# Performance work log

Measured on AMD Instinct MI355X. Metric: run time of the kernel, lower is better.

## Reference

```python
import jax, jax.numpy as jnp
import numpy as np

# dims
B, LP, CIN, AUX = 8, 1024, 64, 32
COUT, OUT_LEN = 64, 512
DM, DI, NS, PH, NH = 1024, 2048, 16, 64, 32  # d_model, d_inner, d_state, headdim, n_heads
NL, PATCH, KPRE, KCONV = 4, 8, 5, 4
GG, KH, CHUNK = 8, 2048, 64  # kan grid, kan hidden, chunk_size
DIN = 2 * DI + 2 * NS + NH   # in_proj output: z, xBC, dt
CONV_DIM = DI + 2 * NS


def _conv1d(x, w, b, stride, pad_l, pad_r, groups=1):
    # x: [B, C, L], w: [O, I/groups, K]
    y = jax.lax.conv_general_dilated(x, w, (stride,), [(pad_l, pad_r)],
                                     dimension_numbers=("NCH", "OIH", "NCH"),
                                     feature_group_count=groups)
    return y + b[None, :, None]


def _rmsnorm(x, w):
    return x * jax.lax.rsqrt(jnp.mean(x * x, axis=-1, keepdims=True) + 1e-5) * w


def _mamba(u, in_w, conv_w, conv_b, A_log, Dh, dt_bias, out_w):
    # Mamba2-style selective SSM block (bias-free projections, causal depthwise conv).
    Bs, L, _ = u.shape
    zxbcdt = jnp.einsum("bld,ed->ble", u, in_w)  # [B,L,DIN]
    z = zxbcdt[..., :DI]
    xBC = zxbcdt[..., DI:DI + CONV_DIM]
    dt = jax.nn.softplus(zxbcdt[..., DI + CONV_DIM:] + dt_bias)  # [B,L,NH]
    xBC = jax.nn.silu(_conv1d(xBC.transpose(0, 2, 1), conv_w, conv_b, 1, KCONV - 1, 0,
                              groups=CONV_DIM)).transpose(0, 2, 1)
    xh = xBC[..., :DI].reshape(Bs, L, NH, PH)
    Bm = xBC[..., DI:DI + NS]   # [B,L,NS]
    Cm = xBC[..., DI + NS:]     # [B,L,NS]
    dA = jnp.exp(-jnp.exp(A_log) * dt)  # [B,L,NH]

    def step(s, t):
        x_t, B_t, C_t, dA_t, dt_t = t
        s = s * dA_t[:, :, None, None] + jnp.einsum("bhp,bn,bh->bhpn", x_t, B_t, dt_t)
        return s, jnp.einsum("bhpn,bn->bhp", s, C_t)

    s0 = jnp.zeros((Bs, NH, PH, NS), u.dtype)
    xs = (xh.transpose(1, 0, 2, 3), Bm.transpose(1, 0, 2), Cm.transpose(1, 0, 2),
          dA.transpose(1, 0, 2), dt.transpose(1, 0, 2))
    _, ys = jax.lax.scan(step, s0, xs)  # ys: [L,B,NH,PH]
    y = ys.transpose(1, 0, 2, 3) + xh * Dh[None, None, :, None]
    y = y.reshape(Bs, L, DI) * jax.nn.silu(z)
    return jnp.einsum("ble,de->bld", y, out_w)


def _kan(x, log_bw, base_w, base_b, spline_w):
    # Gaussian-basis KAN layer: base Linear + spline Linear over RBF expansion.
    grid = jnp.linspace(-2.0, 2.0, GG)
    bw = jnp.exp(log_bw)[None] + 1e-6                 # [1,in,1]
    basis = jnp.exp(-((x[..., None] - grid[None, None, :]) ** 2) / (2.0 * bw * bw))
    return x @ base_w.T + base_b + basis.reshape(x.shape[0], -1) @ spline_w.T


def setup_inputs() -> dict:
    ks = iter(jax.random.split(jax.random.key(0), 64))
    nrm = lambda shape, s=0.02: jax.random.normal(next(ks), shape, jnp.float32) * s
    inp = {"x_prefix": jax.random.normal(next(ks), (B, LP, CIN), jnp.float32),
           "y_aux": jax.random.normal(next(ks), (B, AUX), jnp.float32),
           "pre_conv_w": nrm((DM, CIN, KPRE), 0.1), "pre_conv_b": jnp.zeros((DM,)),
           "patch_w": nrm((DM, DM, PATCH), 0.05), "patch_b": jnp.zeros((DM,))}
    for pre in ("fwd", "bwd"):
        inp[pre + "_norm_w"] = jnp.ones((NL, DM))
        inp[pre + "_in_w"] = nrm((NL, DIN, DM))
        inp[pre + "_conv_w"] = nrm((NL, CONV_DIM, 1, KCONV), 0.1)
        inp[pre + "_conv_b"] = jnp.zeros((NL, CONV_DIM))
        inp[pre + "_A_log"] = jnp.zeros((NL, NH))
        inp[pre + "_D"] = jnp.ones((NL, NH))
        inp[pre + "_dt_bias"] = nrm((NL, NH), 0.5)
        inp[pre + "_out_w"] = nrm((NL, DM, DI))
    inp.update(aux_w=nrm((DM, AUX)), aux_b=jnp.zeros((DM,)),
               kan1_log_bw=jnp.zeros((3 * DM, 1)), kan1_base_w=nrm((KH, 3 * DM)),
               kan1_base_b=jnp.zeros((KH,)), kan1_spline_w=nrm((KH, 3 * DM * GG), 0.005),
               kan2_log_bw=jnp.zeros((KH, 1)), kan2_base_w=nrm((DM, KH)),
               kan2_base_b=jnp.zeros((DM,)), kan2_spline_w=nrm((DM, KH * GG), 0.005),
               shared_w=nrm((DM, DM)), shared_b=jnp.zeros((DM,)),
               heads_w=nrm((COUT, OUT_LEN, DM)), heads_b=jnp.zeros((COUT, OUT_LEN)))
    return inp


def reference(x_prefix, y_aux, pre_conv_w, pre_conv_b, patch_w, patch_b,
              fwd_norm_w, fwd_in_w, fwd_conv_w, fwd_conv_b, fwd_A_log, fwd_D, fwd_dt_bias, fwd_out_w,
              bwd_norm_w, bwd_in_w, bwd_conv_w, bwd_conv_b, bwd_A_log, bwd_D, bwd_dt_bias, bwd_out_w,
              aux_w, aux_b, kan1_log_bw, kan1_base_w, kan1_base_b, kan1_spline_w,
              kan2_log_bw, kan2_base_w, kan2_base_b, kan2_spline_w,
              shared_w, shared_b, heads_w, heads_b):
    # encode_prefix
    x = jax.nn.silu(_conv1d(x_prefix.transpose(0, 2, 1), pre_conv_w, pre_conv_b, 1, KPRE // 2, KPRE // 2))
    x = _conv1d(x, patch_w, patch_b, PATCH, 0, 0).transpose(0, 2, 1)  # [B, 128, DM]
    rem = x.shape[1] % CHUNK
    if rem:
        x = jnp.pad(x, ((0, 0), (0, CHUNK - rem), (0, 0)))
    h_f, h_b = x, x[:, ::-1]
    for i in range(NL):
        h_f = h_f + _mamba(_rmsnorm(h_f, fwd_norm_w[i]), fwd_in_w[i], fwd_conv_w[i], fwd_conv_b[i],
                           fwd_A_log[i], fwd_D[i], fwd_dt_bias[i], fwd_out_w[i])
        h_b = h_b + _mamba(_rmsnorm(h_b, bwd_norm_w[i]), bwd_in_w[i], bwd_conv_w[i], bwd_conv_b[i],
                           bwd_A_log[i], bwd_D[i], bwd_dt_bias[i], bwd_out_w[i])
    ctx = jnp.concatenate([h_f.mean(1), h_b[:, ::-1].mean(1)], axis=-1)  # [B, 2*DM]
    # fusion + heads
    aux = jax.nn.silu(y_aux @ aux_w.T + aux_b)
    fused = jnp.concatenate([ctx, aux], axis=-1)  # [B, 3*DM]
    fused = jax.nn.silu(_kan(fused, kan1_log_bw, kan1_base_w, kan1_base_b, kan1_spline_w))
    fused = jax.nn.silu(_kan(fused, kan2_log_bw, kan2_base_w, kan2_base_b, kan2_spline_w))
    fused = jax.nn.silu(fused @ shared_w.T + shared_b)
    # all channel heads fused into one batched GEMM: [B, OUT_LEN, COUT]
    return jnp.einsum("bd,cld->blc", fused, heads_w) + heads_b.T[None]
```

## Files before the change

### kernel.cpp

```cpp
#include <hip/hip_runtime.h>
#include <hip/hip_bf16.h>
#include <math.h>

#define B_    8
#define LP_   1024
#define CIN_  64
#define DM_   1024
#define DI_   2048
#define NS_   16
#define PH_   64
#define NH_   32
#define NL_   4
#define GG_   8
#define KH_   2048
#define DIN_  4160
#define NPAD_ 4224
#define CONVD_ 2080
#define L_    128
#define R_    1024
#define OUTL_ 512
#define COUT_ 64

typedef __bf16 bf16x8 __attribute__((ext_vector_type(8)));
typedef float f32x4 __attribute__((ext_vector_type(4)));
typedef unsigned short ushort;

__device__ __forceinline__ float silu_f(float x) { return x / (1.0f + expf(-x)); }

__device__ __forceinline__ ushort f2bu(float x) {
    union { __hip_bfloat16 h; ushort u; } c; c.h = __float2bfloat16(x); return c.u;
}
__device__ __forceinline__ float bu2f(ushort u) {
    union { ushort u; __hip_bfloat16 h; } c; c.u = u; return __bfloat162float(c.h);
}

__device__ __forceinline__ void gload_lds16(const void* g, void* l) {
    __builtin_amdgcn_global_load_lds((const __attribute__((address_space(1))) unsigned int*)g,
                                     (__attribute__((address_space(3))) unsigned int*)l, 16, 0, 0);
}

__device__ __forceinline__ float merge2(float a, float b, int mask, int lane) {
    float x = (lane & mask) ? b : a;
    float y = (lane & mask) ? a : b;
    return x + __shfl_xor(y, mask);
}
__device__ __forceinline__ float reduce8(float* a, int lane) {
    float c0 = merge2(a[0], a[1], 1, lane);
    float c1 = merge2(a[2], a[3], 1, lane);
    float c2 = merge2(a[4], a[5], 1, lane);
    float c3 = merge2(a[6], a[7], 1, lane);
    float d0 = merge2(c0, c1, 2, lane);
    float d1 = merge2(c2, c3, 2, lane);
    float e  = merge2(d0, d1, 4, lane);
    e += __shfl_xor(e, 8);
    e += __shfl_xor(e, 16);
    e += __shfl_xor(e, 32);
    return e;
}

#define CVT_IN_T4  1081344
#define CVT_OUT_T4 524288
#define CVT_PER    1605632
#define CVT_TOT    12845056
#define PREP_W1 327680
#define PREP_W2 8388608
#define PREP_W3 2621440
#define PREP_TOT 11337728
__global__ __launch_bounds__(256) void k_cvt_prep(
    const float* __restrict__ in0, const float* __restrict__ in1,
    const float* __restrict__ o0, const float* __restrict__ o1,
    __hip_bfloat16* __restrict__ wBBa, __hip_bfloat16* __restrict__ wOBa,
    const float* __restrict__ pre_w, const float* __restrict__ patch_w, const float* __restrict__ xp,
    __hip_bfloat16* __restrict__ wpreT, __hip_bfloat16* __restrict__ wpatchT, __hip_bfloat16* __restrict__ Apre)
{
    int gi = blockIdx.x * 256 + threadIdx.x;
    if (gi < CVT_TOT) {
        int ld = gi / CVT_PER;
        int r = gi - ld * CVT_PER;
        int l = ld >> 1, d = ld & 1;
        const float* inw  = (d ? in1 : in0) + (size_t)l * DIN_ * DM_;
        const float* outw = (d ? o1 : o0) + (size_t)l * DM_ * DI_;
        if (r < CVT_IN_T4) {
            int idx = r * 4; int row = idx >> 10;
            __hip_bfloat16* dst = wBBa + (size_t)ld * NPAD_ * 1024 + idx;
            if (row < DIN_) {
                float4 v = *(const float4*)(inw + idx);
                dst[0] = __float2bfloat16(v.x); dst[1] = __float2bfloat16(v.y);
                dst[2] = __float2bfloat16(v.z); dst[3] = __float2bfloat16(v.w);
            } else {
                dst[0] = __float2bfloat16(0.f); dst[1] = __float2bfloat16(0.f);
                dst[2] = __float2bfloat16(0.f); dst[3] = __float2bfloat16(0.f);
            }
        } else {
            int idx = (r - CVT_IN_T4) * 4;
            __hip_bfloat16* dst = wOBa + (size_t)ld * 2048 * 1024 + idx;
            float4 v = *(const float4*)(outw + idx);
            dst[0] = __float2bfloat16(v.x); dst[1] = __float2bfloat16(v.y);
            dst[2] = __float2bfloat16(v.z); dst[3] = __float2bfloat16(v.w);
        }
        return;
    }
    int idx = gi - CVT_TOT;
    if (idx < PREP_W1) {
        int d = idx / 320, kk = idx % 320;
        int kp = kk >> 6, c = kk & 63;
        wpreT[idx] = __float2bfloat16(pre_w[(d * CIN_ + c) * 5 + kp]);
    } else if (idx < PREP_W1 + PREP_W2) {
        int i = idx - PREP_W1;
        int d = i >> 13, kk = i & 8191;
        int kp = kk >> 10, din = kk & 1023;
        wpatchT[i] = __float2bfloat16(patch_w[((size_t)d << 13) + din * 8 + kp]);
    } else if (idx < PREP_TOT) {
        int i = idx - PREP_W1 - PREP_W2;
        int kk = i % 320; int r = i / 320;
        int l = r & 1023, b = r >> 10;
        int kp = kk >> 6, c = kk & 63;
        int lp = l + kp - 2;
        float v = 0.f;
        if (lp >= 0 && lp < LP_) v = xp[((size_t)b * LP_ + lp) * CIN_ + c];
        Apre[i] = __float2bfloat16(v);
    }
}

template<int BM, int BN>
__global__ __launch_bounds__(512) void k_gemm_mfma(
    const ushort* __restrict__ A, const ushort* __restrict__ B,
    const float* __restrict__ bias,
    float* __restrict__ Cf, __hip_bfloat16* __restrict__ Cb,
    int Kc, int ldk, int ldc, int Nstore, int act, int nsplit,
    long sA, long sB, long sC)
{
    constexpr int BK = 32;
    constexpr int WM = 64, WN = 32;
    constexpr int MR = WM / 16, NR = WN / 16;
    constexpr int ACH = BM * 4, BCH = BN * 4;
    __shared__ ushort sAs[2][BM * BK];
    __shared__ ushort sBs[2][BN * BK];
    int tid = threadIdx.x;
    int lane = tid & 63, w = tid >> 6;
    int wr = w >> 2, wc = w & 3;
    int z = blockIdx.z;
    int dir = z / nsplit, ks = z - dir * nsplit;
    int kbase = ks * Kc;
    int H = blockIdx.y * gridDim.x + blockIdx.x;
    int nwg = gridDim.x * gridDim.y;
    int chunk = nwg >> 3;
    int Lid = (H & 7) * chunk + (H >> 3);
    int bx = Lid / gridDim.y;
    int by = Lid - bx * gridDim.y;
    int m0 = by * BM, n0 = bx * BN;
    const ushort* Az = A + (size_t)dir * sA + kbase;
    const ushort* Bz = B + (size_t)dir * sB + kbase;

    auto STAGE = [&](int buf, int k0) {
        #pragma unroll
        for (int c = tid; c < ACH; c += 512) {
            int row = c >> 2, gp = c & 3;
            int g = gp ^ ((row >> 1) & 3);
            gload_lds16(Az + (size_t)(m0 + row) * ldk + k0 + g * 8, (char*)&sAs[buf][0] + c * 16);
        }
        #pragma unroll
        for (int c = tid; c < BCH; c += 512) {
            int row = c >> 2, gp = c & 3;
            int g = gp ^ ((row >> 1) & 3);
            gload_lds16(Bz + (size_t)(n0 + row) * ldk + k0 + g * 8, (char*)&sBs[buf][0] + c * 16);
        }
    };

    const int gsw = (((lane >> 4) ^ ((lane >> 1) & 3)) * 8);

    f32x4 acc[MR][NR] = {};
    const int NT = Kc / BK;
    STAGE(0, 0);
    __syncthreads();
    int cur = 0;
    for (int t = 0; t < NT; ++t) {
        if (t + 1 < NT) STAGE(cur ^ 1, (t + 1) * BK);
        bf16x8 af[MR], bfr[NR];
        #pragma unroll
        for (int m = 0; m < MR; ++m)
            af[m] = *(const bf16x8*)&sAs[cur][(wr * WM + m * 16 + (lane & 15)) * BK + gsw];
        #pragma unroll
        for (int n = 0; n < NR; ++n)
            bfr[n] = *(const bf16x8*)&sBs[cur][(wc * WN + n * 16 + (lane & 15)) * BK + gsw];
        #pragma unroll
        for (int m = 0; m < MR; ++m)
            #pragma unroll
            for (int n = 0; n < NR; ++n)
                acc[m][n] = __builtin_amdgcn_mfma_f32_16x16x32_bf16(af[m], bfr[n], acc[m][n], 0, 0, 0);
        __syncthreads();
        cur ^= 1;
    }
    #pragma unroll
    for (int m = 0; m < MR; ++m) {
        int row = m0 + wr * WM + m * 16 + (lane >> 4) * 4;
        #pragma unroll
        for (int n = 0; n < NR; ++n) {
            int col = n0 + wc * WN + n * 16 + (lane & 15);
            if (col < Nstore) {
                if (act == 2) {
                    float* Cfz = Cf + (size_t)z * sC;
                    #pragma unroll
                    for (int j = 0; j < 4; ++j)
                        Cfz[(size_t)(row + j) * ldc + col] = acc[m][n][j];
                } else {
                    __hip_bfloat16* Cbz = Cb + (size_t)dir * sC;
                    float bv = bias ? bias[col] : 0.f;
                    #pragma unroll
                    for (int j = 0; j < 4; ++j) {
                        float v = acc[m][n][j] + bv;
                        if (act == 1) v = silu_f(v);
                        Cbz[(size_t)(row + j) * ldc + col] = __float2bfloat16(v);
                    }
                }
            }
        }
    }
}

__global__ __launch_bounds__(256) void k_patch_fin_rms(const float* __restrict__ part, const float* __restrict__ bias,
                                                       const float* __restrict__ w0, const float* __restrict__ w1,
                                                       float* __restrict__ hf, float* __restrict__ hb,
                                                       __hip_bfloat16* __restrict__ uB) {
    int r = blockIdx.x;
    int t = threadIdx.x;
    int c = t * 4;
    float4 o = *(const float4*)(bias + c);
    #pragma unroll
    for (int s = 0; s < 8; ++s) {
        float4 v = *(const float4*)(part + (size_t)s * 1048576 + ((size_t)r << 10) + c);
        o.x += v.x; o.y += v.y; o.z += v.z; o.w += v.w;
    }
    *(float4*)(hf + ((size_t)r << 10) + c) = o;
    int rb = r ^ 127;
    *(float4*)(hb + ((size_t)rb << 10) + c) = o;
    float ss = o.x * o.x + o.y * o.y + o.z * o.z + o.w * o.w;
    #pragma unroll
    for (int of = 32; of; of >>= 1) ss += __shfl_xor(ss, of);
    __shared__ float sred[4];
    if ((t & 63) == 0) sred[t >> 6] = ss;
    __syncthreads();
    float tot = sred[0] + sred[1] + sred[2] + sred[3];
    float scale = rsqrtf(tot * (1.0f / DM_) + 1e-5f);
    float4 wf = *(const float4*)(w0 + c);
    float4 wb = *(const float4*)(w1 + c);
    __hip_bfloat16* uf = uB + ((size_t)r << 10) + c;
    __hip_bfloat16* ub = uB + ((size_t)(1024 + rb) << 10) + c;
    uf[0] = __float2bfloat16(o.x * scale * wf.x); uf[1] = __float2bfloat16(o.y * scale * wf.y);
    uf[2] = __float2bfloat16(o.z * scale * wf.z); uf[3] = __float2bfloat16(o.w * scale * wf.w);
    ub[0] = __float2bfloat16(o.x * scale * wb.x); ub[1] = __float2bfloat16(o.y * scale * wb.y);
    ub[2] = __float2bfloat16(o.z * scale * wb.z); ub[3] = __float2bfloat16(o.w * scale * wb.w);
}

template<bool DO_RMS>
__global__ __launch_bounds__(256) void k_oproj_fin_rms(const float* __restrict__ part,
                                                       const float* __restrict__ w0, const float* __restrict__ w1,
                                                       float* __restrict__ h, __hip_bfloat16* __restrict__ uB) {
    int row = blockIdx.x;
    int t = threadIdx.x;
    int c = t * 4;
    const float* p = part + (size_t)(row >> 10) * 4194304 + (size_t)(row & 1023) * 1024 + c;
    float4 o = *(const float4*)(h + ((size_t)row << 10) + c);
    #pragma unroll
    for (int s = 0; s < 4; ++s) {
        float4 v = *(const float4*)(p + (size_t)s * 1048576);
        o.x += v.x; o.y += v.y; o.z += v.z; o.w += v.w;
    }
    *(float4*)(h + ((size_t)row << 10) + c) = o;
    if (DO_RMS) {
        float ss = o.x * o.x + o.y * o.y + o.z * o.z + o.w * o.w;
        #pragma unroll
        for (int of = 32; of; of >>= 1) ss += __shfl_xor(ss, of);
        __shared__ float sred[4];
        if ((t & 63) == 0) sred[t >> 6] = ss;
        __syncthreads();
        float tot = sred[0] + sred[1] + sred[2] + sred[3];
        float scale = rsqrtf(tot * (1.0f / DM_) + 1e-5f);
        const float* w = (row >> 10) ? w1 : w0;
        float4 wv = *(const float4*)(w + c);
        __hip_bfloat16* u = uB + ((size_t)row << 10) + c;
        u[0] = __float2bfloat16(o.x * scale * wv.x); u[1] = __float2bfloat16(o.y * scale * wv.y);
        u[2] = __float2bfloat16(o.z * scale * wv.z); u[3] = __float2bfloat16(o.w * scale * wv.w);
    }
}

__global__ __launch_bounds__(256) void k_scan(const __hip_bfloat16* __restrict__ zx,
                                              const float* __restrict__ cw0, const float* __restrict__ cw1,
                                              const float* __restrict__ cb0, const float* __restrict__ cb1,
                                              const float* __restrict__ dtb0, const float* __restrict__ dtb1,
                                              const float* __restrict__ al0, const float* __restrict__ al1,
                                              const float* __restrict__ D0, const float* __restrict__ D1,
                                              __hip_bfloat16* __restrict__ ys) {
    __shared__ float xs[L_ * PH_];
    __shared__ float Bsh[L_ * NS_];
    __shared__ float Csh[L_ * NS_];
    __shared__ float dts[L_];
    __shared__ float dAs[L_];
    int bx = blockIdx.x;
    int dir = bx >> 8, b = (bx >> 5) & 7, h = bx & 31;
    const __hip_bfloat16* zxd = zx + (size_t)dir * 1024 * DIN_;
    const float* cw = dir ? cw1 : cw0;
    const float* cb = dir ? cb1 : cb0;
    const float* dt_bias = dir ? dtb1 : dtb0;
    const float* A_log   = dir ? al1 : al0;
    const float* Dh      = dir ? D1 : D0;
    __hip_bfloat16* ysd  = ys + (size_t)dir * 1024 * DI_;
    int t = threadIdx.x;
    for (int i = t; i < 2048; i += 256) {
        int l = i >> 4, p4 = i & 15;
        int cc = h * PH_ + p4 * 4;
        float a0 = cb[cc + 0], a1 = cb[cc + 1], a2 = cb[cc + 2], a3 = cb[cc + 3];
        #pragma unroll
        for (int k = 0; k < 4; ++k) {
            int lp = l - 3 + k;
            if (lp >= 0) {
                ushort4 raw = *(const ushort4*)(zxd + (size_t)(b * L_ + lp) * DIN_ + DI_ + cc);
                a0 += bu2f(raw.x) * cw[(cc + 0) * 4 + k];
                a1 += bu2f(raw.y) * cw[(cc + 1) * 4 + k];
                a2 += bu2f(raw.z) * cw[(cc + 2) * 4 + k];
                a3 += bu2f(raw.w) * cw[(cc + 3) * 4 + k];
            }
        }
        float* xp = &xs[l * PH_ + p4 * 4];
        xp[0] = silu_f(a0); xp[1] = silu_f(a1); xp[2] = silu_f(a2); xp[3] = silu_f(a3);
    }
    for (int i = t; i < 1024; i += 256) {
        int l = i >> 3, q4 = i & 7;
        int cc = DI_ + q4 * 4;
        float a0 = cb[cc + 0], a1 = cb[cc + 1], a2 = cb[cc + 2], a3 = cb[cc + 3];
        #pragma unroll
        for (int k = 0; k < 4; ++k) {
            int lp = l - 3 + k;
            if (lp >= 0) {
                ushort4 raw = *(const ushort4*)(zxd + (size_t)(b * L_ + lp) * DIN_ + DI_ + cc);
                a0 += bu2f(raw.x) * cw[(cc + 0) * 4 + k];
                a1 += bu2f(raw.y) * cw[(cc + 1) * 4 + k];
                a2 += bu2f(raw.z) * cw[(cc + 2) * 4 + k];
                a3 += bu2f(raw.w) * cw[(cc + 3) * 4 + k];
            }
        }
        float r0 = silu_f(a0), r1 = silu_f(a1), r2 = silu_f(a2), r3 = silu_f(a3);
        if (q4 < 4) {
            float* bp = &Bsh[l * NS_ + q4 * 4];
            bp[0] = r0; bp[1] = r1; bp[2] = r2; bp[3] = r3;
        } else {
            float* cp = &Csh[l * NS_ + (q4 - 4) * 4];
            cp[0] = r0; cp[1] = r1; cp[2] = r2; cp[3] = r3;
        }
    }
    if (t < L_) {
        float v = bu2f(*(const ushort*)(zxd + (size_t)(b * L_ + t) * DIN_ + 4128 + h)) + dt_bias[h];
        float sp = v > 20.f ? v : log1pf(expf(v));
        dts[t] = sp;
        dAs[t] = expf(-expf(A_log[h]) * sp);
    }
    __syncthreads();
    int p = t >> 2, n0 = (t & 3) * 4;
    float Dv = Dh[h];
    float s0 = 0.f, s1 = 0.f, s2 = 0.f, s3 = 0.f;
    for (int l = 0; l < L_; ++l) {
        float x = xs[l * 64 + p];
        float dAv = dAs[l];
        float xdt = x * dts[l];
        s0 = s0 * dAv + xdt * Bsh[l * 16 + n0 + 0];
        s1 = s1 * dAv + xdt * Bsh[l * 16 + n0 + 1];
        s2 = s2 * dAv + xdt * Bsh[l * 16 + n0 + 2];
        s3 = s3 * dAv + xdt * Bsh[l * 16 + n0 + 3];
        float cp = s0 * Csh[l * 16 + n0 + 0] + s1 * Csh[l * 16 + n0 + 1]
                 + s2 * Csh[l * 16 + n0 + 2] + s3 * Csh[l * 16 + n0 + 3];
        cp += __shfl_xor(cp, 1);
        cp += __shfl_xor(cp, 2);
        if ((t & 3) == 0) xs[l * 64 + p] = cp + x * Dv;
    }
    __syncthreads();
    for (int i = t; i < L_ * PH_; i += 256) {
        int l = i >> 6, pp = i & 63;
        float z = bu2f(*(const ushort*)(zxd + (size_t)(b * L_ + l) * DIN_ + h * PH_ + pp));
        ysd[((size_t)(b * L_ + l)) * DI_ + h * PH_ + pp] = __float2bfloat16(xs[i] * silu_f(z));
    }
}

__device__ __forceinline__ void emit_basis(float v, float lbw, float* __restrict__ bas, size_t base) {
    float bw = expf(lbw) + 1e-6f;
    float inv = 1.0f / (2.0f * bw * bw);
    #pragma unroll
    for (int g = 0; g < GG_; ++g) {
        float gg = -2.0f + g * (4.0f / 7.0f);
        float df = v - gg;
        bas[base + g] = expf(-df * df * inv);
    }
}

__global__ __launch_bounds__(256) void k_meanctx_aux(const float* __restrict__ hf, const float* __restrict__ hb,
                                                     const float* __restrict__ y_aux, const float* __restrict__ aux_w,
                                                     const float* __restrict__ aux_b, const float* __restrict__ k1_lbw,
                                                     float* __restrict__ fused, float* __restrict__ bas1) {
    int bx = blockIdx.x;
    int t = threadIdx.x;
    if (bx < 64) {
        int b = bx >> 3, ch = bx & 7;
        int d4 = t & 31, lg = t >> 5;
        int d = ch * 128 + d4 * 4;
        float4 sf = {0,0,0,0}, sb = {0,0,0,0};
        for (int l = lg; l < L_; l += 8) {
            float4 a = *(const float4*)(hf + ((size_t)b * L_ + l) * DM_ + d);
            float4 c = *(const float4*)(hb + ((size_t)b * L_ + l) * DM_ + d);
            sf.x += a.x; sf.y += a.y; sf.z += a.z; sf.w += a.w;
            sb.x += c.x; sb.y += c.y; sb.z += c.z; sb.w += c.w;
        }
        __shared__ float rf[8][128], rb[8][128];
        *(float4*)&rf[lg][d4 * 4] = sf;
        *(float4*)&rb[lg][d4 * 4] = sb;
        __syncthreads();
        if (t < 128) {
            float s1 = 0.f, s2 = 0.f;
            #pragma unroll
            for (int g = 0; g < 8; ++g) { s1 += rf[g][t]; s2 += rb[g][t]; }
            s1 *= (1.f / L_); s2 *= (1.f / L_);
            int d1 = ch * 128 + t, d2 = DM_ + ch * 128 + t;
            fused[b * 3072 + d1] = s1;
            fused[b * 3072 + d2] = s2;
            emit_basis(s1, k1_lbw[d1], bas1, ((size_t)b * 3072 + d1) * GG_);
            emit_basis(s2, k1_lbw[d2], bas1, ((size_t)b * 3072 + d2) * GG_);
        }
    } else {
        int j = (bx - 64) * 256 + t;
        if (j >= DM_) return;
        for (int b = 0; b < B_; ++b) {
            float acc = aux_b[j];
            for (int a = 0; a < 32; ++a) acc += y_aux[b * 32 + a] * aux_w[j * 32 + a];
            float v = silu_f(acc);
            int d3 = 2 * DM_ + j;
            fused[b * 3072 + d3] = v;
            emit_basis(v, k1_lbw[d3], bas1, ((size_t)b * 3072 + d3) * GG_);
        }
    }
}

template<int MODE>
__global__ __launch_bounds__(256) void k_dotk(const float* __restrict__ Wsp, const float* __restrict__ Xsp, int Ksp,
                                              const float* __restrict__ Wb, const float* __restrict__ Xb, int Kb,
                                              const float* __restrict__ bias, float* __restrict__ out,
                                              int nsp, int nch, int Dout) {
    __shared__ float sX[8][1024];
    int ch = blockIdx.y;
    bool sp = (ch < nsp);
    const float* W = sp ? Wsp : Wb;
    const float* X = sp ? Xsp : Xb;
    int K = sp ? Ksp : Kb;
    int k0 = (sp ? ch : ch - nsp) * 1024;
    int tid = threadIdx.x;
    for (int i = tid; i < 2048; i += 256) {
        int b = i >> 8, kk = (i & 255) * 4;
        *(float4*)&sX[b][kk] = *(const float4*)(X + (size_t)b * K + k0 + kk);
    }
    __syncthreads();
    int wv = tid >> 6, lane = tid & 63;
    int rowBase = blockIdx.x * 32 + wv * 8;
    for (int j = 0; j < 8; ++j) {
        int row = rowBase + j;
        const float* wr = W + (size_t)row * K + k0;
        float acc[8] = {};
        #pragma unroll
        for (int it = 0; it < 4; ++it) {
            int k = it * 256 + lane * 4;
            float4 wvv = *(const float4*)(wr + k);
            #pragma unroll
            for (int b = 0; b < 8; ++b) {
                float4 xv = *(const float4*)&sX[b][k];
                acc[b] += wvv.x * xv.x + wvv.y * xv.y + wvv.z * xv.z + wvv.w * xv.w;
            }
        }
        float e = reduce8(acc, lane);
        if (lane < 8) {
            if (MODE == 0) {
                out[((size_t)row * nch + ch) * 8 + lane] = e;
            } else if (MODE == 1) {
                out[(size_t)lane * Dout + row] = silu_f(e + bias[row]);
            } else {
                int c = row >> 9, l = row & 511;
                out[((size_t)lane * OUTL_ + l) * COUT_ + c] = e + bias[row];
            }
        }
    }
}

__global__ __launch_bounds__(256) void k_fin1_basis2(const float* __restrict__ partial, const float* __restrict__ bb,
                                                     const float* __restrict__ k2_lbw,
                                                     float* __restrict__ k1, float* __restrict__ bas2) {
    int row = blockIdx.x * 256 + threadIdx.x;
    if (row >= 2048) return;
    float bbv = bb[row];
    float lb = expf(k2_lbw[row]) + 1e-6f;
    float inv = 1.0f / (2.0f * lb * lb);
    #pragma unroll
    for (int b = 0; b < 8; ++b) {
        float s = bbv;
        #pragma unroll
        for (int c = 0; c < 27; ++c) s += partial[((size_t)row * 27 + c) * 8 + b];
        float v = silu_f(s);
        k1[(size_t)b * 2048 + row] = v;
        #pragma unroll
        for (int g = 0; g < GG_; ++g) {
            float gg = -2.0f + g * (4.0f / 7.0f);
            float df = v - gg;
            bas2[((size_t)b * 2048 + row) * GG_ + g] = expf(-df * df * inv);
        }
    }
}

template<int NCH>
__global__ __launch_bounds__(256) void k_dot_fin(const float* __restrict__ partial, const float* __restrict__ base_b,
                                                 float* __restrict__ out, int Dout) {
    int row = blockIdx.x * 256 + threadIdx.x;
    if (row >= Dout) return;
    float bb = base_b[row];
    #pragma unroll
    for (int b = 0; b < 8; ++b) {
        float s = bb;
        #pragma unroll
        for (int c = 0; c < NCH; ++c) s += partial[((size_t)row * NCH + c) * 8 + b];
        out[(size_t)b * Dout + row] = silu_f(s);
    }
}

extern "C" void kernel_launch(void* const* d_in, const int* in_sizes, int n_in,
                              void* d_out, int out_size, void* d_ws, size_t ws_size,
                              hipStream_t stream) {
    const float* x_prefix = (const float*)d_in[0];
    const float* y_aux    = (const float*)d_in[1];
    const float* pre_w    = (const float*)d_in[2];
    const float* pre_b    = (const float*)d_in[3];
    const float* patch_w  = (const float*)d_in[4];
    const float* patch_b  = (const float*)d_in[5];
    const float* norm_w[2] = {(const float*)d_in[6],  (const float*)d_in[14]};
    const float* in_w[2]   = {(const float*)d_in[7],  (const float*)d_in[15]};
    const float* conv_w[2] = {(const float*)d_in[8],  (const float*)d_in[16]};
    const float* conv_b[2] = {(const float*)d_in[9],  (const float*)d_in[17]};
    const float* A_log[2]  = {(const float*)d_in[10], (const float*)d_in[18]};
    const float* Dvec[2]   = {(const float*)d_in[11], (const float*)d_in[19]};
    const float* dt_b[2]   = {(const float*)d_in[12], (const float*)d_in[20]};
    const float* out_w[2]  = {(const float*)d_in[13], (const float*)d_in[21]};
    const float* aux_w = (const float*)d_in[22];
    const float* aux_b = (const float*)d_in[23];
    const float* k1_lbw = (const float*)d_in[24];
    const float* k1_bw  = (const float*)d_in[25];
    const float* k1_bb  = (const float*)d_in[26];
    const float* k1_sw  = (const float*)d_in[27];
    const float* k2_lbw = (const float*)d_in[28];
    const float* k2_bw  = (const float*)d_in[29];
    const float* k2_bb  = (const float*)d_in[30];
    const float* k2_sw  = (const float*)d_in[31];
    const float* sh_w = (const float*)d_in[32];
    const float* sh_b = (const float*)d_in[33];
    const float* hw   = (const float*)d_in[34];
    const float* hbias= (const float*)d_in[35];
    float* ws = (float*)d_ws;
    float* out = (float*)d_out;

    const size_t o_ApreB   = 0;
    const size_t o_wpreTB  = 1310720;
    const size_t o_x1B     = 1474560;
    const size_t o_wpatchTB= 5668864;
    const size_t o_uB   = 0;
    const size_t o_zxB  = 1048576;
    const size_t o_ysB  = 5308416;
    const size_t o_hf   = 9863168;
    const size_t o_hb   = 10911744;
    const size_t o_wBBa = 11960320;
    const size_t o_wOBa = 29261824;
    const size_t o_spart= 37650432;
    const size_t total_f = 46039040;
    const size_t o_f1   = 0;
    const size_t o_bas1 = 24576;
    const size_t o_k1   = 221184;
    const size_t o_bas2 = 237568;
    const size_t o_k2   = 368640;
    const size_t o_f4   = 376832;
    const size_t o_part = 385024;
    if (ws_size < total_f * sizeof(float)) return;

    __hip_bfloat16* ApreB   = (__hip_bfloat16*)(ws + o_ApreB);
    __hip_bfloat16* wpreTB  = (__hip_bfloat16*)(ws + o_wpreTB);
    __hip_bfloat16* x1B     = (__hip_bfloat16*)(ws + o_x1B);
    __hip_bfloat16* wpatchTB= (__hip_bfloat16*)(ws + o_wpatchTB);
    __hip_bfloat16* uB      = (__hip_bfloat16*)(ws + o_uB);
    __hip_bfloat16* zxB     = (__hip_bfloat16*)(ws + o_zxB);
    __hip_bfloat16* ysB     = (__hip_bfloat16*)(ws + o_ysB);
    __hip_bfloat16* wBBa    = (__hip_bfloat16*)(ws + o_wBBa);
    __hip_bfloat16* wOBa    = (__hip_bfloat16*)(ws + o_wOBa);
    float* hf = ws + o_hf;
    float* hb = ws + o_hb;

    k_cvt_prep<<<(CVT_TOT + PREP_TOT + 255) / 256, 256, 0, stream>>>(
        in_w[0], in_w[1], out_w[0], out_w[1], wBBa, wOBa,
        pre_w, patch_w, x_prefix, wpreTB, wpatchTB, ApreB);
    k_gemm_mfma<128,128><<<dim3(8, 64, 1), 512, 0, stream>>>(
        (const ushort*)ApreB, (const ushort*)wpreTB, pre_b, nullptr, x1B,
        320, 320, 1024, 1024, 1, 1, 0, 0, 0);
    k_gemm_mfma<128,128><<<dim3(8, 8, 8), 512, 0, stream>>>(
        (const ushort*)x1B, (const ushort*)wpatchTB, nullptr, ws + o_spart, nullptr,
        1024, 8192, 1024, 1024, 2, 8, 0, 0, (long)1024 * 1024);
    k_patch_fin_rms<<<1024, 256, 0, stream>>>(ws + o_spart, patch_b, norm_w[0], norm_w[1], hf, hb, uB);

    for (int i = 0; i < NL_; ++i) {
        k_gemm_mfma<128,128><<<dim3(33, 8, 2), 512, 0, stream>>>(
            (const ushort*)uB, (const ushort*)(wBBa + (size_t)i * 2 * NPAD_ * 1024), nullptr, nullptr, zxB,
            1024, 1024, DIN_, DIN_, 0, 1, (long)1024 * 1024, (long)NPAD_ * 1024, (long)1024 * DIN_);
        k_scan<<<512, 256, 0, stream>>>(zxB,
            conv_w[0] + (size_t)i * CONVD_ * 4, conv_w[1] + (size_t)i * CONVD_ * 4,
            conv_b[0] + (size_t)i * CONVD_, conv_b[1] + (size_t)i * CONVD_,
            dt_b[0] + i * NH_, dt_b[1] + i * NH_, A_log[0] + i * NH_, A_log[1] + i * NH_,
            Dvec[0] + i * NH_, Dvec[1] + i * NH_, ysB);
        k_gemm_mfma<128,128><<<dim3(8, 8, 8), 512, 0, stream>>>(
            (const ushort*)ysB, (const ushort*)(wOBa + (size_t)i * 2 * 2048 * 1024), nullptr, ws + o_spart, nullptr,
            512, 2048, 1024, 1024, 2, 4, (long)1024 * 2048, (long)2048 * 1024, (long)1024 * 1024);
        if (i + 1 < NL_) {
            k_oproj_fin_rms<true><<<2048, 256, 0, stream>>>(ws + o_spart,
                norm_w[0] + (size_t)(i + 1) * DM_, norm_w[1] + (size_t)(i + 1) * DM_, hf, uB);
        } else {
            k_oproj_fin_rms<false><<<2048, 256, 0, stream>>>(ws + o_spart, nullptr, nullptr, hf, nullptr);
        }
    }

    k_meanctx_aux<<<68, 256, 0, stream>>>(hf, hb, y_aux, aux_w, aux_b, k1_lbw, ws + o_f1, ws + o_bas1);
    k_dotk<0><<<dim3(64, 27), 256, 0, stream>>>(k1_sw, ws + o_bas1, 24576, k1_bw, ws + o_f1, 3072,
                                                nullptr, ws + o_part, 24, 27, 2048);
    k_fin1_basis2<<<8, 256, 0, stream>>>(ws + o_part, k1_bb, k2_lbw, ws + o_k1, ws + o_bas2);
    k_dotk<0><<<dim3(32, 18), 256, 0, stream>>>(k2_sw, ws + o_bas2, 16384, k2_bw, ws + o_k1, 2048,
                                                nullptr, ws + o_part, 16, 18, 1024);
    k_dot_fin<18><<<4, 256, 0, stream>>>(ws + o_part, k2_bb, ws + o_k2, 1024);
    k_dotk<1><<<dim3(32, 1), 256, 0, stream>>>(nullptr, nullptr, 0, sh_w, ws + o_k2, 1024,
                                               sh_b, ws + o_f4, 0, 1, 1024);
    k_dotk<2><<<dim3(1024, 1), 256, 0, stream>>>(nullptr, nullptr, 0, hw, ws + o_f4, 1024,
                                                 hbias, out, 0, 1, 32768);
}
```

Measured before the change: 836.3 us.

## Fuse fp32-to-bf16 weight conversion into Mamba projection GEMM B-tile loads

Removes the upfront pass that converted all in_proj and out_proj weights to padded bf16 buffers. The GEMM gains a BF32 mode: B tiles are read as fp32 into registers, bounds-checked against the row count instead of relying on padding, then converted and written to LDS after the MFMAs, overlapping with compute. This drops a large weight read/write pass and cuts workspace, but the GEMMs now read twice the B bytes through registers rather than async global-to-LDS copies.

After: 852.4 us. About the same (+1.9%).

```diff
diff --git a/kernel.cpp b/kernel.cpp
--- a/kernel.cpp
+++ b/kernel.cpp
@@ -14,7 +14,6 @@
 #define GG_   8
 #define KH_   2048
 #define DIN_  4160
-#define NPAD_ 4224
 #define CONVD_ 2080
 #define L_    128
 #define R_    1024
@@ -58,49 +57,15 @@
     return e;
 }
 
-#define CVT_IN_T4  1081344
-#define CVT_OUT_T4 524288
-#define CVT_PER    1605632
-#define CVT_TOT    12845056
 #define PREP_W1 327680
 #define PREP_W2 8388608
 #define PREP_W3 2621440
 #define PREP_TOT 11337728
-__global__ __launch_bounds__(256) void k_cvt_prep(
-    const float* __restrict__ in0, const float* __restrict__ in1,
-    const float* __restrict__ o0, const float* __restrict__ o1,
-    __hip_bfloat16* __restrict__ wBBa, __hip_bfloat16* __restrict__ wOBa,
+__global__ __launch_bounds__(256) void k_prep(
     const float* __restrict__ pre_w, const float* __restrict__ patch_w, const float* __restrict__ xp,
     __hip_bfloat16* __restrict__ wpreT, __hip_bfloat16* __restrict__ wpatchT, __hip_bfloat16* __restrict__ Apre)
 {
-    int gi = blockIdx.x * 256 + threadIdx.x;
-    if (gi < CVT_TOT) {
-        int ld = gi / CVT_PER;
-        int r = gi - ld * CVT_PER;
-        int l = ld >> 1, d = ld & 1;
-        const float* inw  = (d ? in1 : in0) + (size_t)l * DIN_ * DM_;
-        const float* outw = (d ? o1 : o0) + (size_t)l * DM_ * DI_;
-        if (r < CVT_IN_T4) {
-            int idx = r * 4; int row = idx >> 10;
-            __hip_bfloat16* dst = wBBa + (size_t)ld * NPAD_ * 1024 + idx;
-            if (row < DIN_) {
-                float4 v = *(const float4*)(inw + idx);
-                dst[0] = __float2bfloat16(v.x); dst[1] = __float2bfloat16(v.y);
-                dst[2] = __float2bfloat16(v.z); dst[3] = __float2bfloat16(v.w);
-            } else {
-                dst[0] = __float2bfloat16(0.f); dst[1] = __float2bfloat16(0.f);
-                dst[2] = __float2bfloat16(0.f); dst[3] = __float2bfloat16(0.f);
-            }
-        } else {
-            int idx = (r - CVT_IN_T4) * 4;
-            __hip_bfloat16* dst = wOBa + (size_t)ld * 2048 * 1024 + idx;
-            float4 v = *(const float4*)(outw + idx);
-            dst[0] = __float2bfloat16(v.x); dst[1] = __float2bfloat16(v.y);
-            dst[2] = __float2bfloat16(v.z); dst[3] = __float2bfloat16(v.w);
-        }
-        return;
-    }
-    int idx = gi - CVT_TOT;
+    int idx = blockIdx.x * 256 + threadIdx.x;
     if (idx < PREP_W1) {
         int d = idx / 320, kk = idx % 320;
         int kp = kk >> 6, c = kk & 63;
@@ -122,18 +87,18 @@
     }
 }
 
-template<int BM, int BN>
+template<int BM, int BN, int BF32>
 __global__ __launch_bounds__(512) void k_gemm_mfma(
-    const ushort* __restrict__ A, const ushort* __restrict__ B,
+    const ushort* __restrict__ A, const ushort* __restrict__ Bb,
+    const float* __restrict__ Bf0, const float* __restrict__ Bf1,
     const float* __restrict__ bias,
     float* __restrict__ Cf, __hip_bfloat16* __restrict__ Cb,
-    int Kc, int ldk, int ldc, int Nstore, int act, int nsplit,
-    long sA, long sB, long sC)
+    int Kc, int ldkA, int ldkB, int ldc, int Nstore, int act, int nsplit, int Nb,
+    long sA, long sC)
 {
     constexpr int BK = 32;
     constexpr int WM = 64, WN = 32;
     constexpr int MR = WM / 16, NR = WN / 16;
-    constexpr int ACH = BM * 4, BCH = BN * 4;
     __shared__ ushort sAs[2][BM * BK];
     __shared__ ushort sBs[2][BN * BK];
     int tid = threadIdx.x;
@@ -150,32 +115,52 @@
     int by = Lid - bx * gridDim.y;
     int m0 = by * BM, n0 = bx * BN;
     const ushort* Az = A + (size_t)dir * sA + kbase;
-    const ushort* Bz = B + (size_t)dir * sB + kbase;
-
-    auto STAGE = [&](int buf, int k0) {
-        #pragma unroll
-        for (int c = tid; c < ACH; c += 512) {
-            int row = c >> 2, gp = c & 3;
-            int g = gp ^ ((row >> 1) & 3);
-            gload_lds16(Az + (size_t)(m0 + row) * ldk + k0 + g * 8, (char*)&sAs[buf][0] + c * 16);
-        }
-        #pragma unroll
-        for (int c = tid; c < BCH; c += 512) {
-            int row = c >> 2, gp = c & 3;
-            int g = gp ^ ((row >> 1) & 3);
-            gload_lds16(Bz + (size_t)(n0 + row) * ldk + k0 + g * 8, (char*)&sBs[buf][0] + c * 16);
-        }
+    const ushort* Bz = BF32 ? nullptr : (Bb + kbase);
+    const float*  Bfz = BF32 ? ((dir ? Bf1 : Bf0) + kbase) : nullptr;
+
+    const int srow = tid >> 2, sgp = tid & 3;
+    const int sg = sgp ^ ((srow >> 1) & 3);
+    const bool brow_ok = BF32 ? (n0 + srow < Nb) : true;
+
+    auto STAGE_A = [&](int buf, int k0) {
+        gload_lds16(Az + (size_t)(m0 + srow) * ldkA + k0 + sg * 8, (char*)&sAs[buf][0] + tid * 16);
+    };
+    auto STAGE_B16 = [&](int buf, int k0) {
+        gload_lds16(Bz + (size_t)(n0 + srow) * ldkB + k0 + sg * 8, (char*)&sBs[buf][0] + tid * 16);
+    };
+    float4 nb0 = {0,0,0,0}, nb1 = {0,0,0,0};
+    auto LOAD_B32 = [&](int k0) {
+        if (brow_ok) {
+            const float* p = Bfz + (size_t)(n0 + srow) * ldkB + k0 + sg * 8;
+            nb0 = *(const float4*)p;
+            nb1 = *(const float4*)(p + 4);
+        } else { nb0 = {0,0,0,0}; nb1 = {0,0,0,0}; }
+    };
+    auto WRITE_B32 = [&](int buf) {
+        ushort4 p0, p1;
+        p0.x = f2bu(nb0.x); p0.y = f2bu(nb0.y); p0.z = f2bu(nb0.z); p0.w = f2bu(nb0.w);
+        p1.x = f2bu(nb1.x); p1.y = f2bu(nb1.y); p1.z = f2bu(nb1.z); p1.w = f2bu(nb1.w);
+        ushort* dst = (ushort*)((char*)&sBs[buf][0] + tid * 16);
+        *(ushort4*)dst = p0;
+        *(ushort4*)(dst + 4) = p1;
     };
 
     const int gsw = (((lane >> 4) ^ ((lane >> 1) & 3)) * 8);
 
     f32x4 acc[MR][NR] = {};
     const int NT = Kc / BK;
-    STAGE(0, 0);
+    STAGE_A(0, 0);
+    if (BF32) { LOAD_B32(0); WRITE_B32(0); }
+    else      STAGE_B16(0, 0);
     __syncthreads();
     int cur = 0;
     for (int t = 0; t < NT; ++t) {
-        if (t + 1 < NT) STAGE(cur ^ 1, (t + 1) * BK);
+        bool pref = (t + 1 < NT);
+        if (pref) {
+            STAGE_A(cur ^ 1, (t + 1) * BK);
+            if (BF32) LOAD_B32((t + 1) * BK);
+            else      STAGE_B16(cur ^ 1, (t + 1) * BK);
+        }
         bf16x8 af[MR], bfr[NR];
         #pragma unroll
         for (int m = 0; m < MR; ++m)
@@ -188,6 +173,7 @@
             #pragma unroll
             for (int n = 0; n < NR; ++n)
                 acc[m][n] = __builtin_amdgcn_mfma_f32_16x16x32_bf16(af[m], bfr[n], acc[m][n], 0, 0, 0);
+        if (BF32 && pref) WRITE_B32(cur ^ 1);
         __syncthreads();
         cur ^= 1;
     }
@@ -567,10 +553,8 @@
     const size_t o_ysB  = 5308416;
     const size_t o_hf   = 9863168;
     const size_t o_hb   = 10911744;
-    const size_t o_wBBa = 11960320;
-    const size_t o_wOBa = 29261824;
-    const size_t o_spart= 37650432;
-    const size_t total_f = 46039040;
+    const size_t o_spart= 11960320;
+    const size_t total_f = 20348928;
     const size_t o_f1   = 0;
     const size_t o_bas1 = 24576;
     const size_t o_k1   = 221184;
@@ -587,34 +571,35 @@
     __hip_bfloat16* uB      = (__hip_bfloat16*)(ws + o_uB);
     __hip_bfloat16* zxB     = (__hip_bfloat16*)(ws + o_zxB);
     __hip_bfloat16* ysB     = (__hip_bfloat16*)(ws + o_ysB);
-    __hip_bfloat16* wBBa    = (__hip_bfloat16*)(ws + o_wBBa);
-    __hip_bfloat16* wOBa    = (__hip_bfloat16*)(ws + o_wOBa);
     float* hf = ws + o_hf;
     float* hb = ws + o_hb;
 
-    k_cvt_prep<<<(CVT_TOT + PREP_TOT + 255) / 256, 256, 0, stream>>>(
-        in_w[0], in_w[1], out_w[0], out_w[1], wBBa, wOBa,
+    k_prep<<<(PREP_TOT + 255) / 256, 256, 0, stream>>>(
         pre_w, patch_w, x_prefix, wpreTB, wpatchTB, ApreB);
-    k_gemm_mfma<128,128><<<dim3(8, 64, 1), 512, 0, stream>>>(
-        (const ushort*)ApreB, (const ushort*)wpreTB, pre_b, nullptr, x1B,
-        320, 320, 1024, 1024, 1, 1, 0, 0, 0);
-    k_gemm_mfma<128,128><<<dim3(8, 8, 8), 512, 0, stream>>>(
-        (const ushort*)x1B, (const ushort*)wpatchTB, nullptr, ws + o_spart, nullptr,
-        1024, 8192, 1024, 1024, 2, 8, 0, 0, (long)1024 * 1024);
+    k_gemm_mfma<128,128,0><<<dim3(8, 64, 1), 512, 0, stream>>>(
+        (const ushort*)ApreB, (const ushort*)wpreTB, nullptr, nullptr, pre_b, nullptr, x1B,
+        320, 320, 320, 1024, 1024, 1, 1, 1024, 0, 0);
+    k_gemm_mfma<128,128,0><<<dim3(8, 8, 8), 512, 0, stream>>>(
+        (const ushort*)x1B, (const ushort*)wpatchTB, nullptr, nullptr, nullptr, ws + o_spart, nullptr,
+        1024, 8192, 8192, 1024, 1024, 2, 8, 1024, 0, (long)1024 * 1024);
     k_patch_fin_rms<<<1024, 256, 0, stream>>>(ws + o_spart, patch_b, norm_w[0], norm_w[1], hf, hb, uB);
 
     for (int i = 0; i < NL_; ++i) {
-        k_gemm_mfma<128,128><<<dim3(33, 8, 2), 512, 0, stream>>>(
-            (const ushort*)uB, (const ushort*)(wBBa + (size_t)i * 2 * NPAD_ * 1024), nullptr, nullptr, zxB,
-            1024, 1024, DIN_, DIN_, 0, 1, (long)1024 * 1024, (long)NPAD_ * 1024, (long)1024 * DIN_);
+        k_gemm_mfma<128,128,1><<<dim3(33, 8, 2), 512, 0, stream>>>(
+            (const ushort*)uB, nullptr,
+            in_w[0] + (size_t)i * DIN_ * DM_, in_w[1] + (size_t)i * DIN_ * DM_,
+            nullptr, nullptr, zxB,
+            1024, 1024, 1024, DIN_, DIN_, 0, 1, DIN_, (long)1024 * 1024, (long)1024 * DIN_);
         k_scan<<<512, 256, 0, stream>>>(zxB,
             conv_w[0] + (size_t)i * CONVD_ * 4, conv_w[1] + (size_t)i * CONVD_ * 4,
             conv_b[0] + (size_t)i * CONVD_, conv_b[1] + (size_t)i * CONVD_,
             dt_b[0] + i * NH_, dt_b[1] + i * NH_, A_log[0] + i * NH_, A_log[1] + i * NH_,
             Dvec[0] + i * NH_, Dvec[1] + i * NH_, ysB);
-        k_gemm_mfma<128,128><<<dim3(8, 8, 8), 512, 0, stream>>>(
-            (const ushort*)ysB, (const ushort*)(wOBa + (size_t)i * 2 * 2048 * 1024), nullptr, ws + o_spart, nullptr,
-            512, 2048, 1024, 1024, 2, 4, (long)1024 * 2048, (long)2048 * 1024, (long)1024 * 1024);
+        k_gemm_mfma<128,128,1><<<dim3(8, 8, 8), 512, 0, stream>>>(
+            (const ushort*)ysB, nullptr,
+            out_w[0] + (size_t)i * DM_ * DI_, out_w[1] + (size_t)i * DM_ * DI_,
+            nullptr, ws + o_spart, nullptr,
+            512, 2048, 2048, 1024, 1024, 2, 4, 1024, (long)1024 * 2048, (long)1024 * 1024);
         if (i + 1 < NL_) {
             k_oproj_fin_rms<true><<<2048, 256, 0, stream>>>(ws + o_spart,
                 norm_w[0] + (size_t)(i + 1) * DM_, norm_w[1] + (size_t)(i + 1) * DM_, hf, uB);
```
